# Kernel optimization log

Hardware: AMD Instinct MI355X
Metric: run time of the kernel (lower is better)

Reference implementation:

```python
import jax, jax.numpy as jnp
import numpy as np

K = 8
TEMP = 0.05
EPS = 1e-8


def setup_inputs() -> dict:
    key = jax.random.key(0)
    k1, k2, k3, k4, k5, k6 = jax.random.split(key, 6)
    N, D, H = 8192, 1024, 64
    h0 = jax.random.normal(k1, (N, D), dtype=jnp.float32)
    coords = jax.random.uniform(k2, (N, 2), dtype=jnp.float32)
    # tiny MLP params: Linear(2,H) -> ReLU -> Linear(H,1) -> Sigmoid
    W1 = jax.random.normal(k3, (2, H), dtype=jnp.float32) * (1.0 / np.sqrt(2))
    b1 = jnp.zeros((H,), dtype=jnp.float32)
    W2 = jax.random.normal(k4, (H, 1), dtype=jnp.float32) * (1.0 / np.sqrt(H))
    b2 = jnp.zeros((1,), dtype=jnp.float32)
    return {"h0": h0, "coords": coords, "W1": W1, "b1": b1, "W2": W2, "b2": b2}


def reference(h0, coords, W1, b1, W2, b2):
    # pairwise euclidean distances [N, N]
    sq = jnp.sum(coords * coords, axis=-1)                      # [N]
    d2 = sq[:, None] + sq[None, :] - 2.0 * (coords @ coords.T)  # [N, N]
    dist = jnp.sqrt(jnp.maximum(d2, 0.0))

    # k+1 nearest (smallest dist), drop self (index 0)
    _, idx = jax.lax.top_k(-dist, K + 1)                        # [N, K+1]
    knn_idx = idx[:, 1:]                                        # [N, K]

    # gather neighbor features [N, K, D]
    neighbor_feats = h0[knn_idx]

    # cosine similarity between h_i and each neighbor (torch eps semantics)
    num = jnp.einsum('nd,nkd->nk', h0, neighbor_feats)          # [N, K]
    ni = jnp.maximum(jnp.linalg.norm(h0, axis=-1), EPS)         # [N]
    nj = jnp.maximum(jnp.linalg.norm(neighbor_feats, axis=-1), EPS)  # [N, K]
    sim = num / (ni[:, None] * nj)

    # spatial weights from gathered distances
    d_knn = jnp.take_along_axis(dist, knn_idx, axis=1)          # [N, K]
    spatial_w = jnp.exp(-d_knn / TEMP)

    density_input = jnp.stack(
        [sim.mean(axis=1), spatial_w.mean(axis=1)], axis=1)     # [N, 2]

    hmid = jax.nn.relu(density_input @ W1 + b1)
    density = jax.nn.sigmoid(hmid @ W2 + b2)                    # [N, 1]
    return density
```

## Files before the change

### kernel.cpp

```cpp
#include <hip/hip_runtime.h>
#include <math.h>

#define NROWS 8192
#define DIM   1024
#define GRID  64
#define CELLW 0.015625f
#define LPR   16

__device__ __forceinline__ int cell_of(float v) {
    int c = (int)(v * 64.0f);
    return c < 0 ? 0 : (c > 63 ? 63 : c);
}

__device__ __forceinline__ float np_d2(float xi, float yi, float sqi,
                                       float xj, float yj) {
    float sqj = __fadd_rn(__fmul_rn(xj, xj), __fmul_rn(yj, yj));
    float G   = fmaf(yi, yj, __fmul_rn(xi, xj));
    return __fsub_rn(__fadd_rn(sqi, sqj), __fmul_rn(2.0f, G));
}

__global__ __launch_bounds__(256) void norms_kernel(const float* __restrict__ h0,
                                                    float* __restrict__ norms) {
    int gid  = blockIdx.x * blockDim.x + threadIdx.x;
    int wave = gid >> 6;
    int lane = threadIdx.x & 63;
    int nw   = (gridDim.x * blockDim.x) >> 6;
    for (int row = wave; row < NROWS; row += nw) {
        const float4* hp = (const float4*)(h0 + (size_t)row * DIM);
        float acc = 0.f;
#pragma unroll
        for (int t = 0; t < 4; ++t) {
            float4 v = hp[lane + 64 * t];
            acc += v.x * v.x + v.y * v.y + v.z * v.z + v.w * v.w;
        }
#pragma unroll
        for (int off = 32; off >= 1; off >>= 1) acc += __shfl_xor(acc, off, 64);
        if (lane == 0) norms[row] = sqrtf(acc);
    }
}

__global__ __launch_bounds__(1024) void build_grid_kernel(
    const float* __restrict__ coords,
    int* __restrict__ cellStart,
    float4* __restrict__ sxyz) {

    __shared__ int lcnt[4096];
    __shared__ int wsum[16];
    const int t = threadIdx.x;

    for (int i = t; i < 4096; i += 1024) lcnt[i] = 0;
    __syncthreads();

    float2 pc[8]; int pcell[8];
#pragma unroll
    for (int k = 0; k < 8; ++k) {
        int i = t + 1024 * k;
        float2 c = ((const float2*)coords)[i];
        pc[k] = c;
        pcell[k] = cell_of(c.y) * GRID + cell_of(c.x);
        atomicAdd(&lcnt[pcell[k]], 1);
    }
    __syncthreads();

    int c0 = lcnt[t*4+0], c1 = lcnt[t*4+1], c2 = lcnt[t*4+2], c3 = lcnt[t*4+3];
    int s1 = c0, s2 = c0 + c1, s3 = s2 + c2, s4 = s3 + c3;
    int lane = t & 63, wid = t >> 6;
    int inc = s4;
#pragma unroll
    for (int off = 1; off < 64; off <<= 1) {
        int o = __shfl_up(inc, off, 64);
        if (lane >= off) inc += o;
    }
    if (lane == 63) wsum[wid] = inc;
    __syncthreads();
    int wbase = 0;
    for (int w = 0; w < wid; ++w) wbase += wsum[w];
    int excl = wbase + inc - s4;

    cellStart[t*4+0] = excl;
    cellStart[t*4+1] = excl + s1;
    cellStart[t*4+2] = excl + s2;
    cellStart[t*4+3] = excl + s3;
    if (t == 1023) cellStart[4096] = excl + s4;
    lcnt[t*4+0] = excl;
    lcnt[t*4+1] = excl + s1;
    lcnt[t*4+2] = excl + s2;
    lcnt[t*4+3] = excl + s3;
    __syncthreads();

#pragma unroll
    for (int k = 0; k < 8; ++k) {
        int pos = atomicAdd(&lcnt[pcell[k]], 1);
        float x = pc[k].x, y = pc[k].y;
        float sq = __fadd_rn(__fmul_rn(x, x), __fmul_rn(y, y));
        sxyz[pos] = make_float4(x, y, sq, __int_as_float(t + 1024 * k));
    }
}

__global__ __launch_bounds__(256) void knn_kernel(
    const int* __restrict__ cellStart,
    const float4* __restrict__ sxyz,
    unsigned long long* __restrict__ chosen_ws) {

    const int sub = threadIdx.x & (LPR - 1);
    const int g   = (blockIdx.x * 256 + threadIdx.x) / LPR;

    const float4 me = sxyz[g];
    const float xi = me.x, yi = me.y, sqi = me.z;
    const int row = __float_as_int(me.w);
    const int cx = cell_of(xi), cy = cell_of(yi);

    unsigned long long best[10], merged[10];
    int C = 2;
    while (true) {
#pragma unroll
        for (int s = 0; s < 10; ++s) best[s] = ~0ULL;
        int x0 = max(0, cx - C), x1 = min(GRID - 1, cx + C);
        int y0 = max(0, cy - C), y1 = min(GRID - 1, cy + C);
        for (int yy = y0; yy <= y1; ++yy) {
            int s = cellStart[yy * GRID + x0];
            int e = cellStart[yy * GRID + x1 + 1];
            for (int t = s + sub; t < e; t += LPR) {
                float4 c = sxyz[t];
                float d2  = __fsub_rn(__fadd_rn(sqi, c.z),
                                      __fmul_rn(2.0f, fmaf(yi, c.y, __fmul_rn(xi, c.x))));
                float dst = __fsqrt_rn(fmaxf(d2, 0.0f));
                unsigned long long key =
                    ((unsigned long long)__float_as_uint(dst) << 32)
                    | (unsigned int)__float_as_int(c.w);
                if (key < best[9]) {
                    best[9] = key;
#pragma unroll
                    for (int ss = 9; ss >= 1; --ss) {
                        unsigned long long a = best[ss - 1], b = best[ss];
                        unsigned long long lo = a < b ? a : b;
                        unsigned long long hi = a < b ? b : a;
                        best[ss - 1] = lo;
                        best[ss]     = hi;
                    }
                }
            }
        }
#pragma unroll
        for (int r = 0; r < 10; ++r) {
            unsigned long long mn = best[0];
#pragma unroll
            for (int off = 1; off < LPR; off <<= 1) {
                unsigned long long o = __shfl_xor(mn, off, 64);
                mn = (o < mn) ? o : mn;
            }
            if (best[0] == mn) {
#pragma unroll
                for (int ss = 0; ss < 9; ++ss) best[ss] = best[ss + 1];
                best[9] = ~0ULL;
            }
            merged[r] = mn;
        }
        bool done = false;
        if (merged[9] != ~0ULL) {
            float d9 = __uint_as_float((unsigned int)(merged[9] >> 32));
            if (d9 + 1.0e-3f <= (float)C * CELLW) done = true;
        }
        if (done || C >= GRID) break;
        C <<= 1; if (C > GRID) C = GRID;
    }

    if (sub == 0) {
        unsigned long long* o = chosen_ws + (size_t)row * 10;
#pragma unroll
        for (int r = 0; r < 10; ++r) o[r] = merged[r];
    }
}

__global__ __launch_bounds__(256, 1) void gather_final_kernel(
    const float* __restrict__ h0,
    const float* __restrict__ coords,
    const unsigned long long* __restrict__ chosen_ws,
    const float4* __restrict__ sxyz,
    const float* __restrict__ norms,
    const float* __restrict__ W1, const float* __restrict__ b1,
    const float* __restrict__ W2, const float* __restrict__ b2,
    float* __restrict__ out) {

    const int wid  = threadIdx.x >> 6;
    const int lane = threadIdx.x & 63;
    const int bid  = blockIdx.x;
    const int grp  = (bid & 7) * (gridDim.x / 8) + (bid >> 3);
    const int g    = grp * 4 + wid;
    const int row  = __float_as_int(sxyz[g].w);

    const unsigned long long* ch = chosen_ws + (size_t)row * 10;
    unsigned long long chosen[10];
#pragma unroll
    for (int r = 0; r < 10; ++r) chosen[r] = ch[r];

    const float4* hi = (const float4*)(h0 + (size_t)row * DIM);

    float4 av[4];
#pragma unroll
    for (int t = 0; t < 4; ++t) av[t] = hi[lane + 64 * t];

    float4 bv[10][4];
#pragma unroll
    for (int s = 0; s < 10; ++s) {
        const float4* hj =
            (const float4*)(h0 + (size_t)(int)(chosen[s] & 0xFFFFFFFFu) * DIM);
#pragma unroll
        for (int t = 0; t < 4; ++t) bv[s][t] = hj[lane + 64 * t];
    }

    float p[10];
#pragma unroll
    for (int s = 0; s < 10; ++s) p[s] = 0.f;
#pragma unroll
    for (int t = 0; t < 4; ++t) {
#pragma unroll
        for (int s = 0; s < 10; ++s) {
            float4 b = bv[s][t];
            p[s] += av[t].x * b.x + av[t].y * b.y + av[t].z * b.z + av[t].w * b.w;
        }
    }

#pragma unroll
    for (int s = 0; s < 10; ++s) {
        float v = p[s];
#pragma unroll
        for (int off = 1; off < 64; off <<= 1) v += __shfl_xor(v, off, 64);
        p[s] = v;
    }

    const float2 ci = ((const float2*)coords)[row];
    const float xi = ci.x, yi = ci.y;
    const float sqi = __fadd_rn(__fmul_rn(xi, xi), __fmul_rn(yi, yi));

    auto clamped_d2 = [&](unsigned long long key) -> float {
        int j = (int)(key & 0xFFFFFFFFu);
        float2 cj = ((const float2*)coords)[j];
        return fmaxf(np_d2(xi, yi, sqi, cj.x, cj.y), 0.0f);
    };
    const float m0 = clamped_d2(chosen[0]);
    const float m1 = clamped_d2(chosen[1]);
    const float m2 = clamped_d2(chosen[2]);
    const float m8 = clamped_d2(chosen[8]);
    const float m9 = clamped_d2(chosen[9]);

    const float WIN = 2.0e-6f;
    const bool fpair = (m1 - m0) <= WIN;
    const bool ftri  = fpair && ((m2 - m0) <= WIN);
    const bool f89   = (m9 - m8) <= WIN;

    float wd[3];
    wd[0] = ftri ? (1.f / 3.f) : (fpair ? 0.5f : 1.0f);
    wd[1] = ftri ? (1.f / 3.f) : (fpair ? 0.5f : 0.0f);
    wd[2] = ftri ? (1.f / 3.f) : 0.0f;
    const float wc0 = f89 ? 0.5f : 1.0f;
    const float wc1 = f89 ? 0.5f : 0.0f;

    const float ni = fmaxf(norms[row], 1e-8f);

    float sim[10], sw[10];
#pragma unroll
    for (int r = 0; r < 10; ++r) {
        int   j   = (int)(chosen[r] & 0xFFFFFFFFu);
        float dst = __uint_as_float((unsigned int)(chosen[r] >> 32));
        float nj  = fmaxf(norms[j], 1e-8f);
        sim[r] = p[r] / (ni * nj);
        sw[r]  = expf(__fdiv_rn(-dst, 0.05f));
    }

    float Ssim = 0.f, Ssw = 0.f;
#pragma unroll
    for (int r = 0; r < 9; ++r) { Ssim += sim[r]; Ssw += sw[r]; }

    const float w1a = W1[lane], w1b = W1[64 + lane];
    const float b1l = b1[lane], w2l = W2[lane], b2s = b2[0];

    float outacc = 0.f;
#pragma unroll
    for (int d = 0; d < 3; ++d) {
#pragma unroll
        for (int c = 0; c < 2; ++c) {
            float wgt = wd[d] * (c ? wc1 : wc0);
            float simsum = Ssim - sim[d] + (c ? (sim[9] - sim[8]) : 0.f);
            float swsum  = Ssw  - sw[d]  + (c ? (sw[9]  - sw[8])  : 0.f);
            float di0 = simsum * 0.125f;
            float di1 = swsum  * 0.125f;
            float hm = fmaxf(di0 * w1a + di1 * w1b + b1l, 0.f);
            float v  = hm * w2l;
#pragma unroll
            for (int off = 1; off < 64; off <<= 1) v += __shfl_xor(v, off, 64);
            float z = v + b2s;
            outacc += wgt * (1.f / (1.f + expf(-z)));
        }
    }

    if (lane == 0) out[row] = outacc;
}

extern "C" void kernel_launch(void* const* d_in, const int* in_sizes, int n_in,
                              void* d_out, int out_size, void* d_ws, size_t ws_size,
                              hipStream_t stream) {
    const float* h0     = (const float*)d_in[0];
    const float* coords = (const float*)d_in[1];
    const float* W1     = (const float*)d_in[2];
    const float* b1     = (const float*)d_in[3];
    const float* W2     = (const float*)d_in[4];
    const float* b2     = (const float*)d_in[5];
    float* out = (float*)d_out;

    char* ws = (char*)d_ws;
    unsigned long long* chosen_ws = (unsigned long long*)(ws);
    float*  norms     = (float*)(ws + 655360);
    float4* sxyz      = (float4*)(ws + 1015808);
    int*    cellStart = (int*)(ws + 1146880);

    build_grid_kernel  <<<1, 1024, 0, stream>>>(coords, cellStart, sxyz);
    knn_kernel         <<<NROWS * LPR / 256, 256, 0, stream>>>(cellStart, sxyz, chosen_ws);
    norms_kernel       <<<128, 256, 0, stream>>>(h0, norms);
    gather_final_kernel<<<NROWS / 4, 256, 0, stream>>>(h0, coords, chosen_ws, sxyz,
                                                       norms, W1, b1, W2, b2, out);
}
```

Measured before the change: 69.87 us.

## Deduplicate neighbor rows per block and stage them in LDS for reuse

```diff
diff --git a/kernel.cpp b/kernel.cpp
--- a/kernel.cpp
+++ b/kernel.cpp
@@ -6,6 +6,7 @@
 #define GRID  64
 #define CELLW 0.015625f
 #define LPR   16
+#define NCACHE 15
 
 __device__ __forceinline__ int cell_of(float v) {
     int c = (int)(v * 64.0f);
@@ -21,22 +22,18 @@
 
 __global__ __launch_bounds__(256) void norms_kernel(const float* __restrict__ h0,
                                                     float* __restrict__ norms) {
-    int gid  = blockIdx.x * blockDim.x + threadIdx.x;
-    int wave = gid >> 6;
+    int wave = (blockIdx.x * 256 + threadIdx.x) >> 6;
     int lane = threadIdx.x & 63;
-    int nw   = (gridDim.x * blockDim.x) >> 6;
-    for (int row = wave; row < NROWS; row += nw) {
-        const float4* hp = (const float4*)(h0 + (size_t)row * DIM);
-        float acc = 0.f;
-#pragma unroll
-        for (int t = 0; t < 4; ++t) {
-            float4 v = hp[lane + 64 * t];
-            acc += v.x * v.x + v.y * v.y + v.z * v.z + v.w * v.w;
-        }
-#pragma unroll
-        for (int off = 32; off >= 1; off >>= 1) acc += __shfl_xor(acc, off, 64);
-        if (lane == 0) norms[row] = sqrtf(acc);
-    }
+    const float4* hp = (const float4*)(h0 + (size_t)wave * DIM);
+    float acc = 0.f;
+#pragma unroll
+    for (int t = 0; t < 4; ++t) {
+        float4 v = hp[lane + 64 * t];
+        acc += v.x * v.x + v.y * v.y + v.z * v.z + v.w * v.w;
+    }
+#pragma unroll
+    for (int off = 1; off < 64; off <<= 1) acc += __shfl_xor(acc, off, 64);
+    if (lane == 0) norms[wave] = sqrtf(acc);
 }
 
 __global__ __launch_bounds__(1024) void build_grid_kernel(
@@ -172,7 +169,7 @@
     }
 }
 
-__global__ __launch_bounds__(256, 1) void gather_final_kernel(
+__global__ __launch_bounds__(256) void gather_final_kernel(
     const float* __restrict__ h0,
     const float* __restrict__ coords,
     const unsigned long long* __restrict__ chosen_ws,
@@ -182,43 +179,93 @@
     const float* __restrict__ W2, const float* __restrict__ b2,
     float* __restrict__ out) {
 
-    const int wid  = threadIdx.x >> 6;
-    const int lane = threadIdx.x & 63;
+    __shared__ float ldsRows[NCACHE][DIM];
+    __shared__ unsigned long long chLDS[40];
+    __shared__ int slotSrc[40];
+    __shared__ int uniq[NCACHE];
+    __shared__ int ridLDS[4];
+
+    const int t    = threadIdx.x;
+    const int wv   = t >> 6;
+    const int lane = t & 63;
     const int bid  = blockIdx.x;
     const int grp  = (bid & 7) * (gridDim.x / 8) + (bid >> 3);
-    const int g    = grp * 4 + wid;
-    const int row  = __float_as_int(sxyz[g].w);
-
-    const unsigned long long* ch = chosen_ws + (size_t)row * 10;
-    unsigned long long chosen[10];
-#pragma unroll
-    for (int r = 0; r < 10; ++r) chosen[r] = ch[r];
+
+    if (wv == 0) {
+        if (lane < 4) ridLDS[lane] = __float_as_int(sxyz[grp * 4 + lane].w);
+        int rid4 = __shfl(ridLDS[0], 0, 64);
+        (void)rid4;
+        unsigned long long mykey = ~0ULL;
+        int myid = -1;
+        if (lane < 40) {
+            int r = ridLDS[lane / 10];
+            mykey = chosen_ws[(size_t)r * 10 + (lane % 10)];
+            myid  = (int)(mykey & 0xFFFFFFFFu);
+            chLDS[lane] = mykey;
+        }
+        int dupof = -1;
+#pragma unroll 8
+        for (int m = 0; m < 40; ++m) {
+            int idm = __shfl(myid, m, 64);
+            if (dupof < 0 && m < lane && idm == myid) dupof = m;
+        }
+        bool isuniq = (lane < 40) && (dupof < 0);
+        unsigned long long um = __ballot(isuniq);
+        int upos = __popcll(um & ((1ULL << lane) - 1ULL));
+        int srcLane = (dupof < 0) ? lane : dupof;
+        int gotPos  = __shfl(upos, srcLane, 64);
+        if (lane < 40) slotSrc[lane] = (gotPos < NCACHE) ? gotPos : -1;
+        if (isuniq && upos < NCACHE) uniq[upos] = myid;
+        if (lane == 0) {
+            int U = (int)__popcll(um);
+            uniq[0] = (upos == 0 && isuniq) ? myid : uniq[0];
+            slotSrc[0] = slotSrc[0];
+        }
+    }
+    __syncthreads();
+
+    int nU = 0;
+#pragma unroll
+    for (int k = 0; k < 40; ++k) nU = max(nU, slotSrc[k] + 1);
+
+    for (int u = 0; u < nU; ++u) {
+        const float4* src = (const float4*)(h0 + (size_t)uniq[u] * DIM);
+        ((float4*)ldsRows[u])[t] = src[t];
+    }
+    __syncthreads();
+
+    const int row = ridLDS[wv];
+    unsigned long long ck[10];
+#pragma unroll
+    for (int r = 0; r < 10; ++r) ck[r] = chLDS[wv * 10 + r];
 
     const float4* hi = (const float4*)(h0 + (size_t)row * DIM);
-
     float4 av[4];
 #pragma unroll
-    for (int t = 0; t < 4; ++t) av[t] = hi[lane + 64 * t];
-
-    float4 bv[10][4];
+    for (int tt = 0; tt < 4; ++tt) av[tt] = hi[lane + 64 * tt];
+
+    float p[10];
 #pragma unroll
     for (int s = 0; s < 10; ++s) {
-        const float4* hj =
-            (const float4*)(h0 + (size_t)(int)(chosen[s] & 0xFFFFFFFFu) * DIM);
-#pragma unroll
-        for (int t = 0; t < 4; ++t) bv[s][t] = hj[lane + 64 * t];
-    }
-
-    float p[10];
-#pragma unroll
-    for (int s = 0; s < 10; ++s) p[s] = 0.f;
-#pragma unroll
-    for (int t = 0; t < 4; ++t) {
-#pragma unroll
-        for (int s = 0; s < 10; ++s) {
-            float4 b = bv[s][t];
-            p[s] += av[t].x * b.x + av[t].y * b.y + av[t].z * b.z + av[t].w * b.w;
-        }
+        int src = slotSrc[wv * 10 + s];
+        float ps = 0.f;
+        if (src >= 0) {
+            const float4* bp = (const float4*)ldsRows[src];
+#pragma unroll
+            for (int tt = 0; tt < 4; ++tt) {
+                float4 b = bp[lane + 64 * tt];
+                ps += av[tt].x * b.x + av[tt].y * b.y + av[tt].z * b.z + av[tt].w * b.w;
+            }
+        } else {
+            int j = (int)(ck[s] & 0xFFFFFFFFu);
+            const float4* bp = (const float4*)(h0 + (size_t)j * DIM);
+#pragma unroll
+            for (int tt = 0; tt < 4; ++tt) {
+                float4 b = bp[lane + 64 * tt];
+                ps += av[tt].x * b.x + av[tt].y * b.y + av[tt].z * b.z + av[tt].w * b.w;
+            }
+        }
+        p[s] = ps;
     }
 
 #pragma unroll
@@ -238,11 +285,11 @@
         float2 cj = ((const float2*)coords)[j];
         return fmaxf(np_d2(xi, yi, sqi, cj.x, cj.y), 0.0f);
     };
-    const float m0 = clamped_d2(chosen[0]);
-    const float m1 = clamped_d2(chosen[1]);
-    const float m2 = clamped_d2(chosen[2]);
-    const float m8 = clamped_d2(chosen[8]);
-    const float m9 = clamped_d2(chosen[9]);
+    const float m0 = clamped_d2(ck[0]);
+    const float m1 = clamped_d2(ck[1]);
+    const float m2 = clamped_d2(ck[2]);
+    const float m8 = clamped_d2(ck[8]);
+    const float m9 = clamped_d2(ck[9]);
 
     const float WIN = 2.0e-6f;
     const bool fpair = (m1 - m0) <= WIN;
@@ -261,8 +308,8 @@
     float sim[10], sw[10];
 #pragma unroll
     for (int r = 0; r < 10; ++r) {
-        int   j   = (int)(chosen[r] & 0xFFFFFFFFu);
-        float dst = __uint_as_float((unsigned int)(chosen[r] >> 32));
+        int   j   = (int)(ck[r] & 0xFFFFFFFFu);
+        float dst = __uint_as_float((unsigned int)(ck[r] >> 32));
         float nj  = fmaxf(norms[j], 1e-8f);
         sim[r] = p[r] / (ni * nj);
         sw[r]  = expf(__fdiv_rn(-dst, 0.05f));
@@ -316,7 +363,7 @@
 
     build_grid_kernel  <<<1, 1024, 0, stream>>>(coords, cellStart, sxyz);
     knn_kernel         <<<NROWS * LPR / 256, 256, 0, stream>>>(cellStart, sxyz, chosen_ws);
-    norms_kernel       <<<128, 256, 0, stream>>>(h0, norms);
+    norms_kernel       <<<NROWS / 4, 256, 0, stream>>>(h0, norms);
     gather_final_kernel<<<NROWS / 4, 256, 0, stream>>>(h0, coords, chosen_ws, sxyz,
                                                        norms, W1, b1, W2, b2, out);
 }
```

New measurement: 80.03 us. 14.6% more time.
